# Kernel tuning notes

Measured on AMD Instinct MI355X. Metric: run time of the kernel, lower is better.

The kernel has to match this reference:

```python
import jax, jax.numpy as jnp
import numpy as np

DIM = 384
COMP = 64          # mmcv CARAFEPack compressed_channels default
KK = 9             # up_kernel^2 (up_kernel=3)
S = 2              # scale_factor


def conv2d(x, w, b, pad):
    y = jax.lax.conv_general_dilated(
        x, w, window_strides=(1, 1), padding=((pad, pad), (pad, pad)),
        dimension_numbers=('NCHW', 'OIHW', 'NCHW'))
    return y + b[None, :, None, None]


def pixel_shuffle(x, s):
    b, c, h, w = x.shape
    x = x.reshape(b, c // (s * s), s, s, h, w)
    x = x.transpose(0, 1, 4, 2, 5, 3)  # b, c', h, s, w, s
    return x.reshape(b, c // (s * s), h * s, w * s)


def carafe_pack(x, cw, cb, ew, eb):
    # x: [b, c, h, w] -> [b, c, 2h, 2w]
    b, c, h, w = x.shape
    comp = conv2d(x, cw, cb, 0)          # [b, 64, h, w]
    mask = conv2d(comp, ew, eb, 1)       # [b, 36, h, w]
    mask = pixel_shuffle(mask, S)        # [b, 9, 2h, 2w]
    mask = jax.nn.softmax(mask, axis=1)  # normalize the 9 reassembly weights
    # unfold 3x3 neighborhoods of x (zero pad 1)
    xp = jnp.pad(x, ((0, 0), (0, 0), (1, 1), (1, 1)))
    patches = jnp.stack(
        [xp[:, :, di:di + h, dj:dj + w] for di in range(3) for dj in range(3)],
        axis=2)                          # [b, c, 9, h, w]
    # each high-res pixel (i,j) reads the low-res window at (i//2, j//2)
    mr = mask.reshape(b, KK, h, S, w, S)
    out = jnp.einsum('bckhw,bkhpwq->bchpwq', patches, mr)
    return out.reshape(b, c, h * S, w * S)


def bilinear_resize(x, h, w):
    b, c = x.shape[:2]
    return jax.image.resize(x, (b, c, h, w), method='bilinear')


def stage(src, guidance, cw, cb, ew, eb):
    h, w = src.shape[2], src.shape[3]
    g = bilinear_resize(guidance, h, w)
    up = carafe_pack(jnp.concatenate([src, g], axis=1), cw, cb, ew, eb)
    return up[:, :DIM]


def setup_inputs() -> dict:
    key = jax.random.key(0)
    ks = jax.random.split(key, 20)
    cin = DIM + 3
    d = {}
    d['source'] = jax.random.normal(ks[0], (4, DIM, 14, 14), jnp.float32)
    d['guidance'] = jax.random.normal(ks[1], (4, 3, 224, 224), jnp.float32)
    i = 2
    for name in ('up1', 'up2', 'up3', 'up4'):
        d[name + '_cw'] = jax.random.normal(ks[i], (COMP, cin, 1, 1), jnp.float32) / np.sqrt(cin); i += 1
        d[name + '_cb'] = jnp.zeros((COMP,), jnp.float32)
        d[name + '_ew'] = jax.random.normal(ks[i], (KK * S * S, COMP, 3, 3), jnp.float32) / np.sqrt(COMP * 9); i += 1
        d[name + '_eb'] = jnp.zeros((KK * S * S,), jnp.float32)
    d['proj_w'] = jax.random.normal(ks[i], (DIM, cin, 1, 1), jnp.float32) / np.sqrt(cin)
    d['proj_b'] = jnp.zeros((DIM,), jnp.float32)
    return d


def reference(source, guidance,
              up1_cw, up1_cb, up1_ew, up1_eb,
              up2_cw, up2_cb, up2_ew, up2_eb,
              up3_cw, up3_cb, up3_ew, up3_eb,
              up4_cw, up4_cb, up4_ew, up4_eb,
              proj_w, proj_b):
    s2 = stage(source, guidance, up1_cw, up1_cb, up1_ew, up1_eb)
    s4 = stage(s2, guidance, up2_cw, up2_cb, up2_ew, up2_eb)
    s8 = stage(s4, guidance, up3_cw, up3_cb, up3_ew, up3_eb)
    s16 = stage(s8, guidance, up4_cw, up4_cb, up4_ew, up4_eb)
    return conv2d(jnp.concatenate([s16, guidance], axis=1), proj_w, proj_b, 0)
```

## Files before the change

kernel.cpp:

```cpp
#include <hip/hip_runtime.h>
#include <cstdint>

#define BATCH 4
#define DIMC 384
#define CINC 387
#define COMPC 64
#define GSZ 224

typedef __attribute__((ext_vector_type(8))) short bf16x8;
typedef __attribute__((ext_vector_type(4))) short s16x4;
typedef __attribute__((ext_vector_type(4))) float f32x4;

static __device__ __forceinline__ unsigned short f2bf(float x) {
  unsigned int u = __float_as_uint(x);
  unsigned int r = (u + 0x7fffu + ((u >> 16) & 1u)) >> 16;
  return (unsigned short)r;
}
static __device__ __forceinline__ float bf2f(unsigned short b) {
  return __uint_as_float(((unsigned int)b) << 16);
}
static __device__ __forceinline__ void cvt2(float x, unsigned short& h, unsigned short& l) {
  unsigned int u = __float_as_uint(x);
  unsigned int hb = (u + 0x7fffu + ((u >> 16) & 1u)) >> 16;
  h = (unsigned short)hb;
  float r = x - __uint_as_float(hb << 16);
  unsigned int u2 = __float_as_uint(r);
  l = (unsigned short)((u2 + 0x7fffu + ((u2 >> 16) & 1u)) >> 16);
}

__global__ void resize_all(const float* __restrict__ g, float* __restrict__ o0,
                           float* __restrict__ o1, float* __restrict__ o2,
                           float* __restrict__ o3) {
  int s = blockIdx.y;
  int h = 14 << s;
  float* out = (s == 0) ? o0 : (s == 1) ? o1 : (s == 2) ? o2 : o3;
  int inv_scale = GSZ / h;
  int w = h;
  int idx = blockIdx.x * blockDim.x + threadIdx.x;
  int total = BATCH * 3 * h * w;
  if (idx >= total) return;
  int j = idx % w; int t = idx / w;
  int i = t % h; t /= h;
  float ks = (float)inv_scale;
  float sy = (i + 0.5f) * ks - 0.5f;
  float sx = (j + 0.5f) * ks - 0.5f;
  int y0 = (int)ceilf(sy - ks); if (y0 < 0) y0 = 0;
  int y1 = (int)floorf(sy + ks); if (y1 > GSZ - 1) y1 = GSZ - 1;
  int x0 = (int)ceilf(sx - ks); if (x0 < 0) x0 = 0;
  int x1 = (int)floorf(sx + ks); if (x1 > GSZ - 1) x1 = GSZ - 1;
  const float* gp = g + (size_t)t * GSZ * GSZ;
  float wsx = 0.f;
  for (int x = x0; x <= x1; ++x) wsx += fmaxf(0.f, 1.f - fabsf(sx - (float)x) / ks);
  float acc = 0.f, wsy = 0.f;
  for (int y = y0; y <= y1; ++y) {
    float wy = fmaxf(0.f, 1.f - fabsf(sy - (float)y) / ks);
    wsy += wy;
    if (wy > 0.f) {
      const float* rp = gp + (size_t)y * GSZ;
      float row = 0.f;
      for (int x = x0; x <= x1; ++x) {
        float wx = fmaxf(0.f, 1.f - fabsf(sx - (float)x) / ks);
        row += wx * rp[x];
      }
      acc += wy * row;
    }
  }
  out[idx] = acc / (wsx * wsy);
}

__global__ void prep_cw(const float* __restrict__ c0, const float* __restrict__ c1,
                        const float* __restrict__ c2, const float* __restrict__ c3,
                        float* __restrict__ cwT) {
  int s = blockIdx.y;
  const float* cw = (s == 0) ? c0 : (s == 1) ? c1 : (s == 2) ? c2 : c3;
  int idx = blockIdx.x * 256 + threadIdx.x;
  if (idx >= CINC * COMPC) return;
  int ci = idx >> 6, co = idx & 63;
  cwT[s * (CINC * COMPC) + idx] = cw[co * CINC + ci];
}

#define EW2_PER_S (4 * COMPC * 9 * 12)
__global__ void prep_ew(const float* __restrict__ e0, const float* __restrict__ e1,
                        const float* __restrict__ e2, const float* __restrict__ e3,
                        float* __restrict__ ewT2) {
  int s = blockIdx.y;
  const float* ew = (s == 0) ? e0 : (s == 1) ? e1 : (s == 2) ? e2 : e3;
  int idx = blockIdx.x * 256 + threadIdx.x;
  if (idx >= EW2_PER_S) return;
  int k = idx % 12; int r = idx / 12;
  int tap = r % 9; r /= 9;
  int ci = r % COMPC; int pos = r / COMPC;
  float val = 0.f;
  if (k < 9) val = ew[(size_t)(k * 4 + pos) * (COMPC * 9) + ci * 9 + tap];
  ewT2[(size_t)s * EW2_PER_S + idx] = val;
}

#define KPAD 416
__global__ void prep_w(const float* __restrict__ pw, short* __restrict__ Whi,
                       short* __restrict__ Wlo) {
  int idx = blockIdx.x * 256 + threadIdx.x;
  if (idx >= DIMC * KPAD) return;
  int co = idx / KPAD, k = idx % KPAD;
  float v = (k < CINC) ? pw[co * CINC + k] : 0.f;
  unsigned short hb = f2bf(v);
  Whi[idx] = (short)hb;
  Wlo[idx] = (short)f2bf(v - bf2f(hb));
}

__global__ void comp_conv_kernel(const float* __restrict__ src, const float* __restrict__ g,
                                 const float* __restrict__ cwT, const float* __restrict__ cb,
                                 float* __restrict__ comp, int h, int w) {
  int hw = h * w;
  int p = blockIdx.x * 256 + threadIdx.x;
  if (p >= hw) return;
  int co0 = blockIdx.y * 32;
  int n = blockIdx.z;
  float acc[32];
  #pragma unroll
  for (int c = 0; c < 32; ++c) acc[c] = cb[co0 + c];
  const float* sp = src + (size_t)n * DIMC * hw + p;
  const float* wbase = cwT + co0;
  for (int ci = 0; ci < DIMC; ++ci) {
    float v = sp[(size_t)ci * hw];
    const float* wr = wbase + ci * COMPC;
    #pragma unroll
    for (int c = 0; c < 32; c += 4) {
      float4 wv = *(const float4*)(wr + c);
      acc[c] += wv.x * v; acc[c + 1] += wv.y * v;
      acc[c + 2] += wv.z * v; acc[c + 3] += wv.w * v;
    }
  }
  const float* gp = g + (size_t)n * 3 * hw + p;
  #pragma unroll
  for (int ci = 0; ci < 3; ++ci) {
    float v = gp[(size_t)ci * hw];
    const float* wr = wbase + (DIMC + ci) * COMPC;
    #pragma unroll
    for (int c = 0; c < 32; c += 4) {
      float4 wv = *(const float4*)(wr + c);
      acc[c] += wv.x * v; acc[c + 1] += wv.y * v;
      acc[c + 2] += wv.z * v; acc[c + 3] += wv.w * v;
    }
  }
  float* op = comp + (size_t)n * COMPC * hw + p;
  #pragma unroll
  for (int c = 0; c < 32; ++c) op[(size_t)(co0 + c) * hw] = acc[c];
}

__global__ void enc_mask_kernel(const float* __restrict__ comp, const float* __restrict__ ewT2,
                                const float* __restrict__ eb, float* __restrict__ mask,
                                int h, int w) {
  int hw = h * w;
  int sw2 = w >> 1;
  int nstrip = h * sw2;
  int strip = blockIdx.x * 256 + threadIdx.x;
  if (strip >= nstrip) return;
  int pos = blockIdx.y;
  int n = blockIdx.z;
  int i = strip / sw2;
  int j0 = (strip - i * sw2) * 2;
  float acc[2][9];
  #pragma unroll
  for (int k = 0; k < 9; ++k) {
    float bv = eb[k * 4 + pos];
    acc[0][k] = bv; acc[1][k] = bv;
  }
  const float* cpn = comp + (size_t)n * COMPC * hw;
  const float* wpos = ewT2 + (size_t)pos * COMPC * 9 * 12;
  for (int ci = 0; ci < COMPC; ++ci) {
    const float* cp = cpn + (size_t)ci * hw;
    float v[3][4];
    #pragma unroll
    for (int di = 0; di < 3; ++di) {
      int y = i + di - 1;
      bool yok = (y >= 0 && y < h);
      #pragma unroll
      for (int xx = 0; xx < 4; ++xx) {
        int x = j0 - 1 + xx;
        v[di][xx] = (yok && x >= 0 && x < w) ? cp[(size_t)y * w + x] : 0.f;
      }
    }
    const float* wb = wpos + (size_t)ci * 9 * 12;
    #pragma unroll
    for (int tap = 0; tap < 9; ++tap) {
      int di = tap / 3, dj = tap % 3;
      float4 wa = *(const float4*)(wb + tap * 12);
      float4 wc = *(const float4*)(wb + tap * 12 + 4);
      float w8 = wb[tap * 12 + 8];
      #pragma unroll
      for (int px = 0; px < 2; ++px) {
        float val = v[di][dj + px];
        acc[px][0] += wa.x * val; acc[px][1] += wa.y * val;
        acc[px][2] += wa.z * val; acc[px][3] += wa.w * val;
        acc[px][4] += wc.x * val; acc[px][5] += wc.y * val;
        acc[px][6] += wc.z * val; acc[px][7] += wc.w * val;
        acc[px][8] += w8 * val;
      }
    }
  }
  int pp = pos >> 1, q = pos & 1;
  int H = 2 * h, W = 2 * w;
  #pragma unroll
  for (int px = 0; px < 2; ++px) {
    int jj = j0 + px;
    float m = -1e30f;
    #pragma unroll
    for (int k = 0; k < 9; ++k) m = fmaxf(m, acc[px][k]);
    float e[9]; float s = 0.f;
    #pragma unroll
    for (int k = 0; k < 9; ++k) { e[k] = __expf(acc[px][k] - m); s += e[k]; }
    float inv = 1.f / s;
    float* mp = mask + (((size_t)n * H + (2 * i + pp)) * W + (2 * jj + q)) * 9;
    #pragma unroll
    for (int k = 0; k < 9; ++k) mp[k] = e[k] * inv;
  }
}

__global__ void carafe_kernel(const float* __restrict__ src, const float* __restrict__ mask,
                              float* __restrict__ out, int h, int w) {
  int p = blockIdx.x * blockDim.x + threadIdx.x;
  int hw = h * w;
  if (p >= hw) return;
  int c0 = blockIdx.y * 48, n = blockIdx.z;
  int i = p / w, j = p % w;
  int H = 2 * h, W = 2 * w;
  float m[4][9];
  #pragma unroll
  for (int pp = 0; pp < 2; ++pp)
    #pragma unroll
    for (int q = 0; q < 2; ++q) {
      const float* mp = mask + (((size_t)n * H + (2 * i + pp)) * W + (2 * j + q)) * 9;
      #pragma unroll
      for (int k = 0; k < 9; ++k) m[pp * 2 + q][k] = mp[k];
    }
  for (int cc = 0; cc < 48; ++cc) {
    int c = c0 + cc;
    const float* sp = src + ((size_t)(n * DIMC + c)) * hw;
    float v[9];
    #pragma unroll
    for (int k = 0; k < 9; ++k) {
      int y = i - 1 + k / 3, x = j - 1 + k % 3;
      v[k] = (y >= 0 && y < h && x >= 0 && x < w) ? sp[(size_t)y * w + x] : 0.f;
    }
    float* op = out + ((size_t)(n * DIMC + c)) * H * W;
    #pragma unroll
    for (int pp = 0; pp < 2; ++pp) {
      float a0 = 0.f, a1 = 0.f;
      #pragma unroll
      for (int k = 0; k < 9; ++k) {
        a0 += v[k] * m[pp * 2 + 0][k];
        a1 += v[k] * m[pp * 2 + 1][k];
      }
      float2 r; r.x = a0; r.y = a1;
      *(float2*)(op + (size_t)(2 * i + pp) * W + 2 * j) = r;
    }
  }
}

__global__ __launch_bounds__(512, 4) void final_conv_mfma4(
    const float* __restrict__ guid, const short* __restrict__ Whi,
    const short* __restrict__ Wlo, const float* __restrict__ pb,
    float* __restrict__ out) {
  __shared__ short XH[2][2048];
  __shared__ short XL[2][2048];
  const int HW = GSZ * GSZ;
  const int n = blockIdx.y;
  const int px0 = blockIdx.x * 64;
  const int tid = threadIdx.x;
  const int wv = tid >> 6;
  const int lane = tid & 63;
  const int lm = lane & 15, qq = lane >> 4;

  const int s_nt = lane >> 4, s_lm = lane & 15;
  const int s_qq = wv >> 1;
  const int s_jh = (wv & 1) * 4;
  const int waddr = ((s_nt * 4 + s_qq) * 16 + s_lm) * 8 + s_jh;

  const float* Xb = out + (size_t)n * DIMC * HW + px0 + lane;
  const float* Gb = guid + (size_t)n * 3 * HW + px0 + lane;

  f32x4 acc[3][4];
  #pragma unroll
  for (int mt = 0; mt < 3; ++mt)
    #pragma unroll
    for (int nt = 0; nt < 4; ++nt) acc[mt][nt] = (f32x4){0.f, 0.f, 0.f, 0.f};

  float nvA[4];
  bf16x8 ahC[3], alC[3];
  {
    unsigned short hs[4], ls[4];
    #pragma unroll
    for (int i = 0; i < 4; ++i) {
      float v = Xb[(size_t)(wv * 4 + i) * HW];
      cvt2(v, hs[i], ls[i]);
    }
    *(s16x4*)&XH[0][waddr] = (s16x4){(short)hs[0], (short)hs[1], (short)hs[2], (short)hs[3]};
    *(s16x4*)&XL[0][waddr] = (s16x4){(short)ls[0], (short)ls[1], (short)ls[2], (short)ls[3]};
    #pragma unroll
    for (int i = 0; i < 4; ++i) nvA[i] = Xb[(size_t)(32 + wv * 4 + i) * HW];
    #pragma unroll
    for (int mt = 0; mt < 3; ++mt) {
      int co = wv * 48 + mt * 16 + lm;
      size_t woff = (size_t)co * KPAD + qq * 8;
      ahC[mt] = *(const bf16x8*)(Whi + woff);
      alC[mt] = *(const bf16x8*)(Wlo + woff);
    }
  }
  __syncthreads();

  #pragma unroll
  for (int kt = 0; kt < 13; ++kt) {
    const int cur = kt & 1;
    bf16x8 ahN[3], alN[3];
    if (kt < 12) {
      #pragma unroll
      for (int mt = 0; mt < 3; ++mt) {
        int co = wv * 48 + mt * 16 + lm;
        size_t woff = (size_t)co * KPAD + (kt + 1) * 32 + qq * 8;
        ahN[mt] = *(const bf16x8*)(Whi + woff);
        alN[mt] = *(const bf16x8*)(Wlo + woff);
      }
    }
    float nvB[4] = {0.f, 0.f, 0.f, 0.f};
    if (kt <= 10) {
      int kb = (kt + 2) * 32 + wv * 4;
      if (kt < 10) {
        #pragma unroll
        for (int i = 0; i < 4; ++i) nvB[i] = Xb[(size_t)(kb + i) * HW];
      } else {
        #pragma unroll
        for (int i = 0; i < 4; ++i) {
          int k = kb + i;
          nvB[i] = (k < CINC) ? Gb[(size_t)(k - DIMC) * HW] : 0.f;
        }
      }
    }
    #pragma unroll
    for (int nt = 0; nt < 4; ++nt) {
      int a = ((nt * 4 + qq) * 16 + lm) * 8;
      bf16x8 bh = *(const bf16x8*)&XH[cur][a];
      bf16x8 bl = *(const bf16x8*)&XL[cur][a];
      #pragma unroll
      for (int mt = 0; mt < 3; ++mt) {
        acc[mt][nt] = __builtin_amdgcn_mfma_f32_16x16x32_bf16(ahC[mt], bh, acc[mt][nt], 0, 0, 0);
        acc[mt][nt] = __builtin_amdgcn_mfma_f32_16x16x32_bf16(ahC[mt], bl, acc[mt][nt], 0, 0, 0);
        acc[mt][nt] = __builtin_amdgcn_mfma_f32_16x16x32_bf16(alC[mt], bh, acc[mt][nt], 0, 0, 0);
      }
    }
    if (kt <= 11) {
      unsigned short hs[4], ls[4];
      #pragma unroll
      for (int i = 0; i < 4; ++i) cvt2(nvA[i], hs[i], ls[i]);
      *(s16x4*)&XH[cur ^ 1][waddr] = (s16x4){(short)hs[0], (short)hs[1], (short)hs[2], (short)hs[3]};
      *(s16x4*)&XL[cur ^ 1][waddr] = (s16x4){(short)ls[0], (short)ls[1], (short)ls[2], (short)ls[3]};
    }
    asm volatile("s_waitcnt lgkmcnt(0)" ::: "memory");
    __builtin_amdgcn_s_barrier();
    __builtin_amdgcn_sched_barrier(0);
    #pragma unroll
    for (int i = 0; i < 4; ++i) nvA[i] = nvB[i];
    if (kt < 12) {
      #pragma unroll
      for (int mt = 0; mt < 3; ++mt) { ahC[mt] = ahN[mt]; alC[mt] = alN[mt]; }
    }
  }

  #pragma unroll
  for (int mt = 0; mt < 3; ++mt) {
    #pragma unroll
    for (int nt = 0; nt < 4; ++nt) {
      #pragma unroll
      for (int r = 0; r < 4; ++r) {
        int co = wv * 48 + mt * 16 + qq * 4 + r;
        int px = px0 + nt * 16 + lm;
        out[((size_t)(n * DIMC + co)) * HW + px] = acc[mt][nt][r] + pb[co];
      }
    }
  }
}

extern "C" void kernel_launch(void* const* d_in, const int* in_sizes, int n_in,
                              void* d_out, int out_size, void* d_ws, size_t ws_size,
                              hipStream_t stream) {
  const float* source   = (const float*)d_in[0];
  const float* guidance = (const float*)d_in[1];
  const float* cw[4] = {(const float*)d_in[2],  (const float*)d_in[6],
                        (const float*)d_in[10], (const float*)d_in[14]};
  const float* cb[4] = {(const float*)d_in[3],  (const float*)d_in[7],
                        (const float*)d_in[11], (const float*)d_in[15]};
  const float* ew[4] = {(const float*)d_in[4],  (const float*)d_in[8],
                        (const float*)d_in[12], (const float*)d_in[16]};
  const float* eb[4] = {(const float*)d_in[5],  (const float*)d_in[9],
                        (const float*)d_in[13], (const float*)d_in[17]};
  const float* pw = (const float*)d_in[18];
  const float* pb = (const float*)d_in[19];
  float* out = (float*)d_out;

  float* ws = (float*)d_ws;
  float* g14  = ws;
  float* g28  = g14 + 2352;
  float* g56  = g28 + 9408;
  float* g112 = g56 + 37632;
  float* comp_buf = g112 + 150528;
  float* mask_buf = comp_buf + 3211264;
  float* s2  = mask_buf + 1806336;
  float* s4  = s2 + 1204224;
  float* s8  = s4 + 4816896;
  float* cwT = s8 + 19267584;
  float* ewT2 = cwT + 99072;
  short* Whi = (short*)(ewT2 + 110592);
  short* Wlo = Whi + DIMC * KPAD;

  prep_cw<<<dim3((CINC * COMPC + 255) / 256, 4), 256, 0, stream>>>(cw[0], cw[1], cw[2], cw[3], cwT);
  prep_ew<<<dim3((EW2_PER_S + 255) / 256, 4), 256, 0, stream>>>(ew[0], ew[1], ew[2], ew[3], ewT2);
  prep_w<<<(DIMC * KPAD + 255) / 256, 256, 0, stream>>>(pw, Whi, Wlo);
  resize_all<<<dim3((BATCH * 3 * 112 * 112 + 255) / 256, 4), 256, 0, stream>>>(
      guidance, g14, g28, g56, g112);

  const float* srcs[4] = {source, s2, s4, s8};
  float* outs[4] = {s2, s4, s8, out};
  float* gbufs[4] = {g14, g28, g56, g112};
  const int hs[4] = {14, 28, 56, 112};
  for (int s = 0; s < 4; ++s) {
    int h = hs[s], w = h, hw = h * w;
    int sw2 = w / 2;
    comp_conv_kernel<<<dim3((hw + 255) / 256, 2, BATCH), 256, 0, stream>>>(
        srcs[s], gbufs[s], cwT + s * (CINC * COMPC), cb[s], comp_buf, h, w);
    enc_mask_kernel<<<dim3((h * sw2 + 255) / 256, 4, BATCH), 256, 0, stream>>>(
        comp_buf, ewT2 + (size_t)s * EW2_PER_S, eb[s], mask_buf, h, w);
    carafe_kernel<<<dim3((hw + 255) / 256, DIMC / 48, BATCH), 256, 0, stream>>>(
        srcs[s], mask_buf, outs[s], h, w);
  }
  final_conv_mfma4<<<dim3((GSZ * GSZ) / 64, BATCH), 512, 0, stream>>>(guidance, Whi, Wlo, pb, out);
}
```

Baseline: 1.644 ms.

## Fuse last-stage CARAFE reassembly into the final projection MFMA kernel

The fourth-stage CARAFE kernel no longer writes the full 384-channel 224x224 intermediate to global memory. Instead, the final 1x1 projection kernel computes the reassembled pixels on the fly. It stages low-res s8 tiles in shared memory, applies the per-pixel 9-tap mask, and converts the result into bf16 hi/lo operands for the MFMA GEMM. This removes a large write and reread of the intermediate. In exchange, blocks grow to 1024 threads with more shared memory, and weight fragments are reloaded each k-step without prefetch.

```diff
diff --git a/kernel.cpp b/kernel.cpp
--- a/kernel.cpp
+++ b/kernel.cpp
@@ -257,27 +257,61 @@
   }
 }
 
-__global__ __launch_bounds__(512, 4) void final_conv_mfma4(
+__global__ __launch_bounds__(1024, 4) void fused_carafe_final(
+    const float* __restrict__ s8, const float* __restrict__ mask,
     const float* __restrict__ guid, const short* __restrict__ Whi,
     const short* __restrict__ Wlo, const float* __restrict__ pb,
     float* __restrict__ out) {
-  __shared__ short XH[2][2048];
-  __shared__ short XL[2][2048];
+  __shared__ __align__(16) short XH[2][4096];
+  __shared__ __align__(16) short XL[2][4096];
+  __shared__ __align__(16) float SB[2][2592];
+
   const int HW = GSZ * GSZ;
   const int n = blockIdx.y;
-  const int px0 = blockIdx.x * 64;
+  const int tx = blockIdx.x % 7, ty = blockIdx.x / 7;
+  const int lj0 = tx * 16, li0 = ty * 2;
+  const int Jh0 = tx * 32, Ih0 = ty * 4;
   const int tid = threadIdx.x;
+  const int lane = tid & 63;
   const int wv = tid >> 6;
-  const int lane = tid & 63;
   const int lm = lane & 15, qq = lane >> 4;
-
-  const int s_nt = lane >> 4, s_lm = lane & 15;
-  const int s_qq = wv >> 1;
-  const int s_jh = (wv & 1) * 4;
-  const int waddr = ((s_nt * 4 + s_qq) * 16 + s_lm) * 8 + s_jh;
-
-  const float* Xb = out + (size_t)n * DIMC * HW + px0 + lane;
-  const float* Gb = guid + (size_t)n * 3 * HW + px0 + lane;
+  const int co_sl = wv >> 1, px_sl = wv & 1;
+
+  const int P = tid & 127;
+  const int kq = tid >> 7;
+  const int I_loc = P >> 5, J_loc = P & 31;
+  const int i_loc = I_loc >> 1, j_loc = J_loc >> 1;
+  const int xaddr = (((P >> 4) * 4 + (kq >> 1)) * 16 + (P & 15)) * 8 + (kq & 1) * 4;
+
+  float m9[9];
+  {
+    const float* mp = mask + (((size_t)n * GSZ + (Ih0 + I_loc)) * GSZ + (Jh0 + J_loc)) * 9;
+    #pragma unroll
+    for (int k = 0; k < 9; ++k) m9[k] = mp[k];
+  }
+  float gv[3] = {0.f, 0.f, 0.f};
+  if (kq == 0) {
+    #pragma unroll
+    for (int g = 0; g < 3; ++g)
+      gv[g] = guid[((size_t)(n * 3 + g) * GSZ + (Ih0 + I_loc)) * GSZ + (Jh0 + J_loc)];
+  }
+
+  const float* s8n = s8 + (size_t)n * DIMC * 112 * 112;
+
+  int g_off[3], sb_off[3];
+  bool inr[3], img[3];
+  #pragma unroll
+  for (int r = 0; r < 3; ++r) {
+    int idx = tid + (r << 10);
+    inr[r] = idx < 2304;
+    int idc = inr[r] ? idx : 0;
+    int seg = idc / 18, col = idc - seg * 18;
+    int ch = seg >> 2, row = seg & 3;
+    int y = li0 - 1 + row, x = lj0 - 1 + col;
+    img[r] = (y >= 0 && y < 112 && x >= 0 && x < 112);
+    g_off[r] = (ch * 112 + (img[r] ? y : 0)) * 112 + (img[r] ? x : 0);
+    sb_off[r] = (row * 18 + col) * 36 + ch;
+  }
 
   f32x4 acc[3][4];
   #pragma unroll
@@ -285,84 +319,92 @@
     #pragma unroll
     for (int nt = 0; nt < 4; ++nt) acc[mt][nt] = (f32x4){0.f, 0.f, 0.f, 0.f};
 
-  float nvA[4];
-  bf16x8 ahC[3], alC[3];
+  auto carafe_produce = [&](int bb) {
+    float a0 = 0.f, a1 = 0.f, a2 = 0.f, a3 = 0.f;
+    #pragma unroll
+    for (int tap = 0; tap < 9; ++tap) {
+      int di = tap / 3, dj = tap % 3;
+      float4 s4 = *(const float4*)&SB[bb][((i_loc + di) * 18 + (j_loc + dj)) * 36 + kq * 4];
+      a0 += s4.x * m9[tap];
+      a1 += s4.y * m9[tap];
+      a2 += s4.z * m9[tap];
+      a3 += s4.w * m9[tap];
+    }
+    unsigned short h0, l0, h1, l1, h2, l2, h3, l3;
+    cvt2(a0, h0, l0); cvt2(a1, h1, l1); cvt2(a2, h2, l2); cvt2(a3, h3, l3);
+    *(s16x4*)&XH[bb][xaddr] = (s16x4){(short)h0, (short)h1, (short)h2, (short)h3};
+    *(s16x4*)&XL[bb][xaddr] = (s16x4){(short)l0, (short)l1, (short)l2, (short)l3};
+  };
+
   {
-    unsigned short hs[4], ls[4];
-    #pragma unroll
-    for (int i = 0; i < 4; ++i) {
-      float v = Xb[(size_t)(wv * 4 + i) * HW];
-      cvt2(v, hs[i], ls[i]);
-    }
-    *(s16x4*)&XH[0][waddr] = (s16x4){(short)hs[0], (short)hs[1], (short)hs[2], (short)hs[3]};
-    *(s16x4*)&XL[0][waddr] = (s16x4){(short)ls[0], (short)ls[1], (short)ls[2], (short)ls[3]};
-    #pragma unroll
-    for (int i = 0; i < 4; ++i) nvA[i] = Xb[(size_t)(32 + wv * 4 + i) * HW];
-    #pragma unroll
-    for (int mt = 0; mt < 3; ++mt) {
-      int co = wv * 48 + mt * 16 + lm;
-      size_t woff = (size_t)co * KPAD + qq * 8;
-      ahC[mt] = *(const bf16x8*)(Whi + woff);
-      alC[mt] = *(const bf16x8*)(Wlo + woff);
-    }
+    float v[3];
+    #pragma unroll
+    for (int r = 0; r < 3; ++r)
+      v[r] = (inr[r] && img[r]) ? s8n[g_off[r]] : 0.f;
+    #pragma unroll
+    for (int r = 0; r < 3; ++r)
+      if (inr[r]) SB[0][sb_off[r]] = v[r];
   }
   __syncthreads();
-
-  #pragma unroll
+  {
+    float v[3];
+    const float* sc = s8n + (size_t)32 * 112 * 112;
+    #pragma unroll
+    for (int r = 0; r < 3; ++r)
+      v[r] = (inr[r] && img[r]) ? sc[g_off[r]] : 0.f;
+    carafe_produce(0);
+    #pragma unroll
+    for (int r = 0; r < 3; ++r)
+      if (inr[r]) SB[1][sb_off[r]] = v[r];
+  }
+  __syncthreads();
+
+  #pragma unroll 1
   for (int kt = 0; kt < 13; ++kt) {
     const int cur = kt & 1;
-    bf16x8 ahN[3], alN[3];
-    if (kt < 12) {
-      #pragma unroll
-      for (int mt = 0; mt < 3; ++mt) {
-        int co = wv * 48 + mt * 16 + lm;
-        size_t woff = (size_t)co * KPAD + (kt + 1) * 32 + qq * 8;
-        ahN[mt] = *(const bf16x8*)(Whi + woff);
-        alN[mt] = *(const bf16x8*)(Wlo + woff);
-      }
-    }
-    float nvB[4] = {0.f, 0.f, 0.f, 0.f};
+    bf16x8 ah[3], al[3];
+    #pragma unroll
+    for (int mt = 0; mt < 3; ++mt) {
+      int co = co_sl * 48 + mt * 16 + lm;
+      size_t woff = (size_t)co * KPAD + kt * 32 + qq * 8;
+      ah[mt] = *(const bf16x8*)(Whi + woff);
+      al[mt] = *(const bf16x8*)(Wlo + woff);
+    }
+    float sv[3] = {0.f, 0.f, 0.f};
+    if (kt <= 9) {
+      const float* sc = s8n + (size_t)(kt + 2) * 32 * 112 * 112;
+      #pragma unroll
+      for (int r = 0; r < 3; ++r)
+        if (inr[r] && img[r]) sv[r] = sc[g_off[r]];
+    }
     if (kt <= 10) {
-      int kb = (kt + 2) * 32 + wv * 4;
-      if (kt < 10) {
-        #pragma unroll
-        for (int i = 0; i < 4; ++i) nvB[i] = Xb[(size_t)(kb + i) * HW];
-      } else {
-        #pragma unroll
-        for (int i = 0; i < 4; ++i) {
-          int k = kb + i;
-          nvB[i] = (k < CINC) ? Gb[(size_t)(k - DIMC) * HW] : 0.f;
-        }
-      }
+      carafe_produce(cur ^ 1);
+    } else if (kt == 11) {
+      float a0 = gv[0], a1 = gv[1], a2 = gv[2];
+      unsigned short h0, l0, h1, l1, h2, l2;
+      cvt2(a0, h0, l0); cvt2(a1, h1, l1); cvt2(a2, h2, l2);
+      if (kq != 0) { h0 = l0 = h1 = l1 = h2 = l2 = 0; }
+      *(s16x4*)&XH[0][xaddr] = (s16x4){(short)h0, (short)h1, (short)h2, 0};
+      *(s16x4*)&XL[0][xaddr] = (s16x4){(short)l0, (short)l1, (short)l2, 0};
     }
     #pragma unroll
     for (int nt = 0; nt < 4; ++nt) {
-      int a = ((nt * 4 + qq) * 16 + lm) * 8;
+      int a = (((px_sl * 4 + nt) * 4 + qq) * 16 + lm) * 8;
       bf16x8 bh = *(const bf16x8*)&XH[cur][a];
       bf16x8 bl = *(const bf16x8*)&XL[cur][a];
       #pragma unroll
       for (int mt = 0; mt < 3; ++mt) {
-        acc[mt][nt] = __builtin_amdgcn_mfma_f32_16x16x32_bf16(ahC[mt], bh, acc[mt][nt], 0, 0, 0);
-        acc[mt][nt] = __builtin_amdgcn_mfma_f32_16x16x32_bf16(ahC[mt], bl, acc[mt][nt], 0, 0, 0);
-        acc[mt][nt] = __builtin_amdgcn_mfma_f32_16x16x32_bf16(alC[mt], bh, acc[mt][nt], 0, 0, 0);
-      }
-    }
-    if (kt <= 11) {
-      unsigned short hs[4], ls[4];
-      #pragma unroll
-      for (int i = 0; i < 4; ++i) cvt2(nvA[i], hs[i], ls[i]);
-      *(s16x4*)&XH[cur ^ 1][waddr] = (s16x4){(short)hs[0], (short)hs[1], (short)hs[2], (short)hs[3]};
-      *(s16x4*)&XL[cur ^ 1][waddr] = (s16x4){(short)ls[0], (short)ls[1], (short)ls[2], (short)ls[3]};
-    }
-    asm volatile("s_waitcnt lgkmcnt(0)" ::: "memory");
-    __builtin_amdgcn_s_barrier();
-    __builtin_amdgcn_sched_barrier(0);
-    #pragma unroll
-    for (int i = 0; i < 4; ++i) nvA[i] = nvB[i];
-    if (kt < 12) {
-      #pragma unroll
-      for (int mt = 0; mt < 3; ++mt) { ahC[mt] = ahN[mt]; alC[mt] = alN[mt]; }
-    }
+        acc[mt][nt] = __builtin_amdgcn_mfma_f32_16x16x32_bf16(ah[mt], bh, acc[mt][nt], 0, 0, 0);
+        acc[mt][nt] = __builtin_amdgcn_mfma_f32_16x16x32_bf16(ah[mt], bl, acc[mt][nt], 0, 0, 0);
+        acc[mt][nt] = __builtin_amdgcn_mfma_f32_16x16x32_bf16(al[mt], bh, acc[mt][nt], 0, 0, 0);
+      }
+    }
+    if (kt <= 9) {
+      #pragma unroll
+      for (int r = 0; r < 3; ++r)
+        if (inr[r]) SB[cur][sb_off[r]] = sv[r];
+    }
+    if (kt < 12) __syncthreads();
   }
 
   #pragma unroll
@@ -371,9 +413,10 @@
     for (int nt = 0; nt < 4; ++nt) {
       #pragma unroll
       for (int r = 0; r < 4; ++r) {
-        int co = wv * 48 + mt * 16 + qq * 4 + r;
-        int px = px0 + nt * 16 + lm;
-        out[((size_t)(n * DIMC + co)) * HW + px] = acc[mt][nt][r] + pb[co];
+        int co = co_sl * 48 + mt * 16 + qq * 4 + r;
+        int px = px_sl * 64 + nt * 16 + lm;
+        int I = Ih0 + (px >> 5), J = Jh0 + (px & 31);
+        out[((size_t)(n * DIMC + co)) * HW + (size_t)I * GSZ + J] = acc[mt][nt][r] + pb[co];
       }
     }
   }
@@ -428,8 +471,10 @@
         srcs[s], gbufs[s], cwT + s * (CINC * COMPC), cb[s], comp_buf, h, w);
     enc_mask_kernel<<<dim3((h * sw2 + 255) / 256, 4, BATCH), 256, 0, stream>>>(
         comp_buf, ewT2 + (size_t)s * EW2_PER_S, eb[s], mask_buf, h, w);
-    carafe_kernel<<<dim3((hw + 255) / 256, DIMC / 48, BATCH), 256, 0, stream>>>(
-        srcs[s], mask_buf, outs[s], h, w);
-  }
-  final_conv_mfma4<<<dim3((GSZ * GSZ) / 64, BATCH), 512, 0, stream>>>(guidance, Whi, Wlo, pb, out);
-}
+    if (s < 3)
+      carafe_kernel<<<dim3((hw + 255) / 256, DIMC / 48, BATCH), 256, 0, stream>>>(
+          srcs[s], mask_buf, outs[s], h, w);
+  }
+  fused_carafe_final<<<dim3(392, BATCH), 1024, 0, stream>>>(
+      s8, mask_buf, guidance, Whi, Wlo, pb, out);
+}
```

Result: slower. 1.700 ms (+3.4%).
